# Kernel tuning notes

Hardware: AMD Instinct MI355X
Metric: run time of the kernel (lower is better)

The kernel has to match this reference:

```python
import jax, jax.numpy as jnp
import numpy as np

D = 1024
K = 8
EPS_BN = 1e-5
EPS_L2 = 1e-8


def l2norm(x, axis=-1):
    return x / (jnp.sqrt(jnp.sum(x * x, axis=axis, keepdims=True)) + EPS_L2)


def setup_inputs() -> dict:
    key = jax.random.key(0)
    ks = jax.random.split(key, 12)
    B, T = 256, 72
    H = D // K
    s1 = 1.0 / np.sqrt(D)
    s2 = 1.0 / np.sqrt(H)
    return {
        "img_embed": jax.random.normal(ks[0], (B, 36, D), dtype=jnp.float32),
        "cap_embed": jax.random.normal(ks[1], (B, T, D), dtype=jnp.float32),
        "lens": jax.random.randint(ks[2], (B,), 1, T + 1),
        # fc_gamma: Linear(D,H) -> ReLU -> Linear(H,D); weights stored (in,out)
        "Wg1": jax.random.uniform(ks[3], (D, H), jnp.float32, -s1, s1),
        "bg1": jax.random.uniform(ks[4], (H,), jnp.float32, -s1, s1),
        "Wg2": jax.random.uniform(ks[5], (H, D), jnp.float32, -s2, s2),
        "bg2": jax.random.uniform(ks[6], (D,), jnp.float32, -s2, s2),
        # fc_beta
        "Wb1": jax.random.uniform(ks[7], (D, H), jnp.float32, -s1, s1),
        "bb1": jax.random.uniform(ks[8], (H,), jnp.float32, -s1, s1),
        "Wb2": jax.random.uniform(ks[9], (H, D), jnp.float32, -s2, s2),
        "bb2": jax.random.uniform(ks[10], (D,), jnp.float32, -s2, s2),
    }


def reference(img_embed, cap_embed, lens, Wg1, bg1, Wg2, bg2, Wb1, bb1, Wb2, bb2):
    # img_embed: (B, 36, D), cap_embed: (B, T, D), lens: (B,)
    B, T, _ = cap_embed.shape

    # img_repr: mean over 36 regions -> (B, D)
    img_repr = img_embed.mean(axis=1)

    # BatchNorm1d (affine=False, training): stats over (batch, time) per feature.
    # cap in torch is (B, D, T); stats reduce over batch+time axes.
    mean = cap_embed.mean(axis=(0, 1))                      # (D,)
    var = jnp.mean((cap_embed - mean) ** 2, axis=(0, 1))    # biased, (D,)
    norm_feat = (cap_embed - mean) / jnp.sqrt(var + EPS_BN)  # (B, T, D)

    # Masked mean pooling over valid timesteps (BN stats precede masking,
    # matching the original). Pooling is linear, so conditional affine
    # (gamma,beta constant over time) commutes with it.
    mask = (jnp.arange(T)[None, :] < lens[:, None]).astype(cap_embed.dtype)  # (B, T)
    pooled = jnp.einsum('btd,bt->bd', norm_feat, mask) / lens[:, None].astype(cap_embed.dtype)  # (B_cap, D)

    # Conditional gamma/beta per image
    gammas = jax.nn.relu(img_repr @ Wg1 + bg1) @ Wg2 + bg2   # (B_img, D)
    betas = jax.nn.relu(img_repr @ Wb1 + bb1) @ Wb2 + bb2    # (B_img, D)

    # txt[i, j, :] = pooled[j] * (gamma_i + 1) + beta_i
    txt = pooled[None, :, :] * (gammas[:, None, :] + 1.0) + betas[:, None, :]  # (B_img, B_cap, D)
    txt_n = l2norm(txt, axis=-1)
    img_n = l2norm(img_repr, axis=-1)                        # (B_img, D)

    # sim for image i over captions j; original writes sims[:, i] = sim
    sim_ij = jnp.einsum('id,ijd->ij', img_n, txt_n)          # (B_img, B_cap)
    return sim_ij.T                                          # sims[j, i]
```

## Files before the change

### kernel.cpp

```cpp
#include <hip/hip_runtime.h>
#include <math.h>

#define NDIM 1024
#define HDIM 128
#define NB 256
#define NT 72
#define NR 36
#define KS 16

__device__ __forceinline__ float wave_sum(float v) {
#pragma unroll
  for (int off = 32; off > 0; off >>= 1) v += __shfl_down(v, off, 64);
  return v;
}

__device__ __forceinline__ float dot4(const float4 a, const float4 b) {
  return a.x * b.x + a.y * b.y + a.z * b.z + a.w * b.w;
}

__global__ __launch_bounds__(256) void k_front(const float* __restrict__ img,
                                               const float* __restrict__ cap,
                                               const int* __restrict__ lens,
                                               float* __restrict__ fs, float* __restrict__ fq,
                                               float* __restrict__ ms, float* __restrict__ repr,
                                               float* __restrict__ imgn) {
  const int bid = blockIdx.x, tid = threadIdx.x;
  __shared__ float red[4];
  __shared__ float sInv;
  if (bid < 512) {
    const int b = bid & 255;
    const int half = bid >> 8;
    const int len = lens[b];
    const int t0 = half * 36;
    const float* base = cap + (size_t)b * NT * NDIM + (size_t)t0 * NDIM + tid * 4;
    float fsx = 0.f, fsy = 0.f, fsz = 0.f, fsw = 0.f;
    float fqx = 0.f, fqy = 0.f, fqz = 0.f, fqw = 0.f;
    float msx = 0.f, msy = 0.f, msz = 0.f, msw = 0.f;
#pragma unroll 12
    for (int tt = 0; tt < 36; ++tt) {
      const float4 v = *reinterpret_cast<const float4*>(base + tt * NDIM);
      fsx += v.x; fsy += v.y; fsz += v.z; fsw += v.w;
      fqx += v.x * v.x; fqy += v.y * v.y; fqz += v.z * v.z; fqw += v.w * v.w;
      if (t0 + tt < len) { msx += v.x; msy += v.y; msz += v.z; msw += v.w; }
    }
    const int o = (half * NB + b) * NDIM + tid * 4;
    *reinterpret_cast<float4*>(fs + o) = make_float4(fsx, fsy, fsz, fsw);
    *reinterpret_cast<float4*>(fq + o) = make_float4(fqx, fqy, fqz, fqw);
    *reinterpret_cast<float4*>(ms + o) = make_float4(msx, msy, msz, msw);
  } else {
    const int b = bid - 512;
    const float* base = img + (size_t)b * NR * NDIM + tid * 4;
    float sx = 0.f, sy = 0.f, sz = 0.f, sw = 0.f;
#pragma unroll 12
    for (int r = 0; r < NR; ++r) {
      const float4 v = *reinterpret_cast<const float4*>(base + r * NDIM);
      sx += v.x; sy += v.y; sz += v.z; sw += v.w;
    }
    const float inv = 1.0f / (float)NR;
    sx *= inv; sy *= inv; sz *= inv; sw *= inv;
    *reinterpret_cast<float4*>(repr + (size_t)b * NDIM + tid * 4) = make_float4(sx, sy, sz, sw);
    const float sq = wave_sum(sx * sx + sy * sy + sz * sz + sw * sw);
    const int lane = tid & 63, wv = tid >> 6;
    if (lane == 0) red[wv] = sq;
    __syncthreads();
    if (tid == 0) sInv = 1.0f / (sqrtf(red[0] + red[1] + red[2] + red[3]) + 1e-8f);
    __syncthreads();
    const float iv = sInv;
    *reinterpret_cast<float4*>(imgn + (size_t)b * NDIM + tid * 4) =
        make_float4(sx * iv, sy * iv, sz * iv, sw * iv);
  }
}

__global__ __launch_bounds__(512) void k_mid(const float* __restrict__ fs,
                                             const float* __restrict__ fq,
                                             const float* __restrict__ ms,
                                             const int* __restrict__ lens,
                                             const float* __restrict__ repr,
                                             const float* __restrict__ Wg1,
                                             const float* __restrict__ Wb1,
                                             float* __restrict__ pooled,
                                             float* __restrict__ hpart) {
  const int bid = blockIdx.x, tid = threadIdx.x;
  __shared__ float ss[8][64], sq2[8][64], smu[64], srs[64];
  __shared__ float shr[8][128];
  __shared__ float sacc[8][128][8];
  if (bid < 16) {
    const int d0 = bid * 64, dloc = tid & 63, grp = tid >> 6;
    float s = 0.f, q = 0.f;
    const int r0 = grp * 64;
#pragma unroll 8
    for (int r = r0; r < r0 + 64; ++r) {
      s += fs[(size_t)r * NDIM + d0 + dloc];
      q += fq[(size_t)r * NDIM + d0 + dloc];
    }
    ss[grp][dloc] = s;
    sq2[grp][dloc] = q;
    __syncthreads();
    if (tid < 64) {
      float S = 0.f, Q = 0.f;
#pragma unroll
      for (int g2 = 0; g2 < 8; ++g2) { S += ss[g2][tid]; Q += sq2[g2][tid]; }
      const float invN = 1.0f / (float)(NB * NT);
      const float mu = S * invN;
      const float var = Q * invN - mu * mu;
      smu[tid] = mu;
      srs[tid] = 1.0f / sqrtf(var + 1e-5f);
    }
    __syncthreads();
    const int dcol = tid & 63, brow = tid >> 6;
    const float mu = smu[dcol], rs = srs[dcol];
#pragma unroll 4
    for (int b = brow; b < NB; b += 8) {
      const float invl = 1.0f / (float)lens[b];
      const float m = ms[(size_t)b * NDIM + d0 + dcol] + ms[(size_t)(NB + b) * NDIM + d0 + dcol];
      pooled[(size_t)b * NDIM + d0 + dcol] = (m * invl - mu) * rs;
    }
  } else {
    const int idx = bid - 16;
    const int g = idx & 31, br = (idx >> 5) & 1, ks = idx >> 6;
    const int b0 = g * 8;
    const int kbase = ks * 128;
    const int h2 = tid & 63;
    const int ksub = tid >> 6;
    const float* __restrict__ W = br ? Wb1 : Wg1;
    {
      const int im = tid >> 6, c2 = (tid & 63) * 2;
      *reinterpret_cast<float2*>(&shr[im][c2]) =
          *reinterpret_cast<const float2*>(repr + (size_t)(b0 + im) * NDIM + kbase + c2);
    }
    __syncthreads();
    float acc0[8] = {0, 0, 0, 0, 0, 0, 0, 0}, acc1[8] = {0, 0, 0, 0, 0, 0, 0, 0};
#pragma unroll
    for (int q = 0; q < 4; ++q) {
      const int dl = ksub * 16 + q * 4;
      const float* wq = W + (size_t)(kbase + dl) * HDIM + h2;
      const float wa0 = wq[0], wa1 = wq[128], wa2 = wq[256], wa3 = wq[384];
      const float wb0 = wq[64], wb1 = wq[192], wb2 = wq[320], wb3 = wq[448];
#pragma unroll
      for (int i = 0; i < 8; ++i) {
        const float4 s = *reinterpret_cast<const float4*>(&shr[i][dl]);
        acc0[i] += s.x * wa0 + s.y * wa1 + s.z * wa2 + s.w * wa3;
        acc1[i] += s.x * wb0 + s.y * wb1 + s.z * wb2 + s.w * wb3;
      }
    }
#pragma unroll
    for (int i = 0; i < 8; ++i) {
      sacc[ksub][h2][i] = acc0[i];
      sacc[ksub][h2 + 64][i] = acc1[i];
    }
    __syncthreads();
#pragma unroll
    for (int v = tid; v < 1024; v += 512) {
      const int hh = v & 127, im = v >> 7;
      float s = 0.f;
#pragma unroll
      for (int k2 = 0; k2 < 8; ++k2) s += sacc[k2][hh][im];
      hpart[(((size_t)ks * 2 + br) * NB + b0 + im) * HDIM + hh] = s;
    }
  }
}

__global__ __launch_bounds__(512) void k_l2(
    const float* __restrict__ hpart, const float* __restrict__ bg1,
    const float* __restrict__ bb1, const float* __restrict__ Wg2,
    const float* __restrict__ bg2, const float* __restrict__ Wb2,
    const float* __restrict__ bb2, const float* __restrict__ imgn, float* __restrict__ uarr,
    float* __restrict__ aarr, float* __restrict__ bvarr, float* __restrict__ cpart,
    float* __restrict__ epart) {
  const int gb = blockIdx.x, dgrp = blockIdx.y;
  const int b0 = gb * 8;
  const int tid = threadIdx.x;
  __shared__ float shh[2][8][HDIM];
  __shared__ float sga[8][HDIM];
  __shared__ float sba[8][HDIM];

  {
    const int hh4 = (tid & 31) * 4;
    const int imA = (tid >> 5) & 7;
    const int brA = tid >> 8;
    float4 acc = make_float4(0.f, 0.f, 0.f, 0.f);
    const float* hp = hpart + ((size_t)brA * NB + b0 + imA) * HDIM + hh4;
#pragma unroll
    for (int ks = 0; ks < 8; ++ks) {
      const float4 v = *reinterpret_cast<const float4*>(hp + (size_t)ks * 2 * NB * HDIM);
      acc.x += v.x; acc.y += v.y; acc.z += v.z; acc.w += v.w;
    }
    const float4 bias = *reinterpret_cast<const float4*>((brA ? bb1 : bg1) + hh4);
    *reinterpret_cast<float4*>(&shh[brA][imA][hh4]) =
        make_float4(fmaxf(acc.x + bias.x, 0.f), fmaxf(acc.y + bias.y, 0.f),
                    fmaxf(acc.z + bias.z, 0.f), fmaxf(acc.w + bias.w, 0.f));
  }
  __syncthreads();

  const int dq = tid & 31;
  const int im = (tid >> 5) & 7;
  const int hs = tid >> 8;
  const int d = dgrp * 128 + dq * 4;
  float4 ga = make_float4(0.f, 0.f, 0.f, 0.f), ba = make_float4(0.f, 0.f, 0.f, 0.f);
  const int h0 = hs * 64;
#pragma unroll 8
  for (int h = h0; h < h0 + 64; ++h) {
    const float4 wg = *reinterpret_cast<const float4*>(Wg2 + (size_t)h * NDIM + d);
    const float4 wb = *reinterpret_cast<const float4*>(Wb2 + (size_t)h * NDIM + d);
    const float hg = shh[0][im][h], hb = shh[1][im][h];
    ga.x += hg * wg.x; ga.y += hg * wg.y; ga.z += hg * wg.z; ga.w += hg * wg.w;
    ba.x += hb * wb.x; ba.y += hb * wb.y; ba.z += hb * wb.z; ba.w += hb * wb.w;
  }
  if (hs) {
    *reinterpret_cast<float4*>(&sga[im][dq * 4]) = ga;
    *reinterpret_cast<float4*>(&sba[im][dq * 4]) = ba;
  }
  __syncthreads();
  if (!hs) {
    const float4 g2 = *reinterpret_cast<const float4*>(&sga[im][dq * 4]);
    const float4 b2 = *reinterpret_cast<const float4*>(&sba[im][dq * 4]);
    const float4 bgv = *reinterpret_cast<const float4*>(bg2 + d);
    const float4 bbv = *reinterpret_cast<const float4*>(bb2 + d);
    const float ox = ga.x + g2.x + bgv.x + 1.0f, oy = ga.y + g2.y + bgv.y + 1.0f;
    const float oz = ga.z + g2.z + bgv.z + 1.0f, ow = ga.w + g2.w + bgv.w + 1.0f;
    const float tx = ba.x + b2.x + bbv.x, ty = ba.y + b2.y + bbv.y;
    const float tz = ba.z + b2.z + bbv.z, tw = ba.w + b2.w + bbv.w;
    const size_t o = (size_t)(b0 + im) * NDIM + d;
    const float4 nv = *reinterpret_cast<const float4*>(imgn + o);
    *reinterpret_cast<float4*>(uarr + o) = make_float4(nv.x * ox, nv.y * oy, nv.z * oz, nv.w * ow);
    *reinterpret_cast<float4*>(aarr + o) = make_float4(ox * ox, oy * oy, oz * oz, ow * ow);
    *reinterpret_cast<float4*>(bvarr + o) =
        make_float4(2.0f * ox * tx, 2.0f * oy * ty, 2.0f * oz * tz, 2.0f * ow * tw);
    float c = nv.x * tx + nv.y * ty + nv.z * tz + nv.w * tw;
    float e = tx * tx + ty * ty + tz * tz + tw * tw;
#pragma unroll
    for (int off = 16; off > 0; off >>= 1) {
      c += __shfl_down(c, off, 32);
      e += __shfl_down(e, off, 32);
    }
    if ((tid & 31) == 0) {
      cpart[dgrp * NB + b0 + im] = c;
      epart[dgrp * NB + b0 + im] = e;
    }
  }
}

__global__ __launch_bounds__(256) void k_simtile(
    const float* __restrict__ uarr, const float* __restrict__ aarr,
    const float* __restrict__ bvarr, const float* __restrict__ pooled,
    float* __restrict__ pn, float* __restrict__ pd) {
  __shared__ float su[64][36], sa[64][36], sb[64][36], sp[64][36];
  const int tid = threadIdx.x;
  const int tx = tid & 15, ty = tid >> 4;
  const int i0 = blockIdx.x * 64, j0 = blockIdx.y * 64;
  const int k0 = blockIdx.z * (NDIM / KS);
  const int lr = tid >> 3;
  const int lc = (tid & 7) * 4;
  float an[4][4] = {{0}}, ad[4][4] = {{0}};
  for (int dc = k0; dc < k0 + NDIM / KS; dc += 32) {
    __syncthreads();
#pragma unroll
    for (int rep = 0; rep < 2; ++rep) {
      const int r = lr + rep * 32;
      *reinterpret_cast<float4*>(&su[r][lc]) =
          *reinterpret_cast<const float4*>(uarr + (size_t)(i0 + r) * NDIM + dc + lc);
      *reinterpret_cast<float4*>(&sa[r][lc]) =
          *reinterpret_cast<const float4*>(aarr + (size_t)(i0 + r) * NDIM + dc + lc);
      *reinterpret_cast<float4*>(&sb[r][lc]) =
          *reinterpret_cast<const float4*>(bvarr + (size_t)(i0 + r) * NDIM + dc + lc);
      *reinterpret_cast<float4*>(&sp[r][lc]) =
          *reinterpret_cast<const float4*>(pooled + (size_t)(j0 + r) * NDIM + dc + lc);
    }
    __syncthreads();
#pragma unroll
    for (int dd = 0; dd < 32; dd += 4) {
      float4 rp[4], rq[4];
#pragma unroll
      for (int n = 0; n < 4; ++n) {
        rp[n] = *reinterpret_cast<const float4*>(&sp[ty + 16 * n][dd]);
        rq[n] = make_float4(rp[n].x * rp[n].x, rp[n].y * rp[n].y, rp[n].z * rp[n].z,
                            rp[n].w * rp[n].w);
      }
#pragma unroll
      for (int m = 0; m < 4; ++m) {
        const float4 ru = *reinterpret_cast<const float4*>(&su[tx + 16 * m][dd]);
        const float4 ra = *reinterpret_cast<const float4*>(&sa[tx + 16 * m][dd]);
        const float4 rb = *reinterpret_cast<const float4*>(&sb[tx + 16 * m][dd]);
#pragma unroll
        for (int n = 0; n < 4; ++n) {
          an[m][n] += dot4(ru, rp[n]);
          ad[m][n] += dot4(ra, rq[n]) + dot4(rb, rp[n]);
        }
      }
    }
  }
  const int s = blockIdx.z;
#pragma unroll
  for (int m = 0; m < 4; ++m) {
#pragma unroll
    for (int n = 0; n < 4; ++n) {
      const int i = i0 + tx + 16 * m, j = j0 + ty + 16 * n;
      const size_t o = ((size_t)s * NB + j) * NB + i;
      pn[o] = an[m][n];
      pd[o] = ad[m][n];
    }
  }
}

__global__ __launch_bounds__(256) void k_reduce(const float* __restrict__ pn,
                                                const float* __restrict__ pd,
                                                const float* __restrict__ cpart,
                                                const float* __restrict__ epart,
                                                float* __restrict__ out) {
  const int j = blockIdx.x, i = threadIdx.x;
  const size_t base = (size_t)j * NB + i;
  float n = 0.f, den = 0.f;
#pragma unroll
  for (int s = 0; s < KS; ++s) {
    const size_t o = base + (size_t)s * (NB * NB);
    n += pn[o];
    den += pd[o];
  }
  float cv = 0.f, ev = 0.f;
#pragma unroll
  for (int s = 0; s < 8; ++s) { cv += cpart[s * NB + i]; ev += epart[s * NB + i]; }
  const float num = n + cv;
  const float den2 = den + ev;
  out[base] = num / (sqrtf(fmaxf(den2, 0.0f)) + 1e-8f);
}

extern "C" void kernel_launch(void* const* d_in, const int* in_sizes, int n_in,
                              void* d_out, int out_size, void* d_ws, size_t ws_size,
                              hipStream_t stream) {
  const float* img = (const float*)d_in[0];
  const float* cap = (const float*)d_in[1];
  const int* lens = (const int*)d_in[2];
  const float* Wg1 = (const float*)d_in[3];
  const float* bg1 = (const float*)d_in[4];
  const float* Wg2 = (const float*)d_in[5];
  const float* bg2 = (const float*)d_in[6];
  const float* Wb1 = (const float*)d_in[7];
  const float* bb1 = (const float*)d_in[8];
  const float* Wb2 = (const float*)d_in[9];
  const float* bb2 = (const float*)d_in[10];
  float* out = (float*)d_out;

  float* w = (float*)d_ws;
  float* fullsum = w; w += 2 * NB * NDIM;
  float* fullsq = w;  w += 2 * NB * NDIM;
  float* msum = w;    w += 2 * NB * NDIM;
  float* hpart = w;   w += 16 * NB * HDIM;
  float* pooled = w;  w += NB * NDIM;
  float* uarr = w;    w += NB * NDIM;
  float* aarr = w;    w += NB * NDIM;
  float* bvarr = w;   w += NB * NDIM;
  float* cpart = w;   w += 8 * NB;
  float* epart = w;   w += 8 * NB;
  float* repr = uarr;
  float* imgn = aarr;
  float* pn = fullsum;
  float* pd = msum;

  hipLaunchKernelGGL(k_front, dim3(768), dim3(256), 0, stream, img, cap, lens, fullsum, fullsq,
                     msum, repr, imgn);
  hipLaunchKernelGGL(k_mid, dim3(528), dim3(512), 0, stream, fullsum, fullsq, msum, lens, repr,
                     Wg1, Wb1, pooled, hpart);
  hipLaunchKernelGGL(k_l2, dim3(32, 8), dim3(512), 0, stream, hpart, bg1, bb1, Wg2, bg2, Wb2,
                     bb2, imgn, uarr, aarr, bvarr, cpart, epart);
  hipLaunchKernelGGL(k_simtile, dim3(4, 4, KS), dim3(256), 0, stream, uarr, aarr, bvarr, pooled,
                     pn, pd);
  hipLaunchKernelGGL(k_reduce, dim3(NB), dim3(256), 0, stream, pn, pd, cpart, epart, out);
}
```

Baseline: 76.07 us.

## Reuse second-layer weights across images and retile the similarity kernel with fewer K-splits

The second MLP layer is restructured so each thread loads one weight float4 and applies it to all 8 images of the block. Partial sums over 8 h-segments are reduced through shared memory, which cuts repeated Wg2/Wb2 global loads. The similarity kernel now uses 32x32 tiles with 4 K-splits instead of 64x64 tiles with 16. This keeps the same block count but shrinks the partial-sum buffers the final reduce must read, at the cost of lower register reuse per thread. repr/imgn get their own workspace instead of aliasing uarr/aarr.

```diff
diff --git a/kernel.cpp b/kernel.cpp
--- a/kernel.cpp
+++ b/kernel.cpp
@@ -6,7 +6,7 @@
 #define NB 256
 #define NT 72
 #define NR 36
-#define KS 16
+#define KS 4
 
 __device__ __forceinline__ float wave_sum(float v) {
 #pragma unroll
@@ -171,8 +171,7 @@
   const int b0 = gb * 8;
   const int tid = threadIdx.x;
   __shared__ float shh[2][8][HDIM];
-  __shared__ float sga[8][HDIM];
-  __shared__ float sba[8][HDIM];
+  __shared__ float sacc[2][8][8][HDIM];
 
   {
     const int hh4 = (tid & 31) * 4;
@@ -192,50 +191,59 @@
   }
   __syncthreads();
 
-  const int dq = tid & 31;
-  const int im = (tid >> 5) & 7;
-  const int hs = tid >> 8;
-  const int d = dgrp * 128 + dq * 4;
-  float4 ga = make_float4(0.f, 0.f, 0.f, 0.f), ba = make_float4(0.f, 0.f, 0.f, 0.f);
-  const int h0 = hs * 64;
-#pragma unroll 8
-  for (int h = h0; h < h0 + 64; ++h) {
-    const float4 wg = *reinterpret_cast<const float4*>(Wg2 + (size_t)h * NDIM + d);
-    const float4 wb = *reinterpret_cast<const float4*>(Wb2 + (size_t)h * NDIM + d);
-    const float hg = shh[0][im][h], hb = shh[1][im][h];
-    ga.x += hg * wg.x; ga.y += hg * wg.y; ga.z += hg * wg.z; ga.w += hg * wg.w;
-    ba.x += hb * wb.x; ba.y += hb * wb.y; ba.z += hb * wb.z; ba.w += hb * wb.w;
-  }
-  if (hs) {
-    *reinterpret_cast<float4*>(&sga[im][dq * 4]) = ga;
-    *reinterpret_cast<float4*>(&sba[im][dq * 4]) = ba;
+  {
+    const int dq = tid & 31;
+    const int kseg = (tid >> 5) & 7;
+    const int br = tid >> 8;
+    const int d = dgrp * 128 + dq * 4;
+    const float* __restrict__ W = br ? Wb2 : Wg2;
+    float4 acc[8];
+#pragma unroll
+    for (int im = 0; im < 8; ++im) acc[im] = make_float4(0.f, 0.f, 0.f, 0.f);
+    const int h0 = kseg * 16;
+#pragma unroll
+    for (int hh = 0; hh < 16; ++hh) {
+      const int h = h0 + hh;
+      const float4 w4 = *reinterpret_cast<const float4*>(W + (size_t)h * NDIM + d);
+#pragma unroll
+      for (int im = 0; im < 8; ++im) {
+        const float hv = shh[br][im][h];
+        acc[im].x += hv * w4.x; acc[im].y += hv * w4.y;
+        acc[im].z += hv * w4.z; acc[im].w += hv * w4.w;
+      }
+    }
+#pragma unroll
+    for (int im = 0; im < 8; ++im)
+      *reinterpret_cast<float4*>(&sacc[br][kseg][im][dq * 4]) = acc[im];
   }
   __syncthreads();
-  if (!hs) {
-    const float4 g2 = *reinterpret_cast<const float4*>(&sga[im][dq * 4]);
-    const float4 b2 = *reinterpret_cast<const float4*>(&sba[im][dq * 4]);
-    const float4 bgv = *reinterpret_cast<const float4*>(bg2 + d);
-    const float4 bbv = *reinterpret_cast<const float4*>(bb2 + d);
-    const float ox = ga.x + g2.x + bgv.x + 1.0f, oy = ga.y + g2.y + bgv.y + 1.0f;
-    const float oz = ga.z + g2.z + bgv.z + 1.0f, ow = ga.w + g2.w + bgv.w + 1.0f;
-    const float tx = ba.x + b2.x + bbv.x, ty = ba.y + b2.y + bbv.y;
-    const float tz = ba.z + b2.z + bbv.z, tw = ba.w + b2.w + bbv.w;
-    const size_t o = (size_t)(b0 + im) * NDIM + d;
-    const float4 nv = *reinterpret_cast<const float4*>(imgn + o);
-    *reinterpret_cast<float4*>(uarr + o) = make_float4(nv.x * ox, nv.y * oy, nv.z * oz, nv.w * ow);
-    *reinterpret_cast<float4*>(aarr + o) = make_float4(ox * ox, oy * oy, oz * oz, ow * ow);
-    *reinterpret_cast<float4*>(bvarr + o) =
-        make_float4(2.0f * ox * tx, 2.0f * oy * ty, 2.0f * oz * tz, 2.0f * ow * tw);
-    float c = nv.x * tx + nv.y * ty + nv.z * tz + nv.w * tw;
-    float e = tx * tx + ty * ty + tz * tz + tw * tw;
-#pragma unroll
-    for (int off = 16; off > 0; off >>= 1) {
-      c += __shfl_down(c, off, 32);
-      e += __shfl_down(e, off, 32);
-    }
-    if ((tid & 31) == 0) {
-      cpart[dgrp * NB + b0 + im] = c;
-      epart[dgrp * NB + b0 + im] = e;
+
+  {
+    const int imC = tid >> 6;
+    const int dl = (tid & 63) * 2;
+    float g0 = 0.f, g1 = 0.f, t0 = 0.f, t1 = 0.f;
+#pragma unroll
+    for (int ks = 0; ks < 8; ++ks) {
+      g0 += sacc[0][ks][imC][dl];
+      g1 += sacc[0][ks][imC][dl + 1];
+      t0 += sacc[1][ks][imC][dl];
+      t1 += sacc[1][ks][imC][dl + 1];
+    }
+    const int d = dgrp * 128 + dl;
+    const float2 bgv = *reinterpret_cast<const float2*>(bg2 + d);
+    const float2 bbv = *reinterpret_cast<const float2*>(bb2 + d);
+    const float ox0 = g0 + bgv.x + 1.0f, ox1 = g1 + bgv.y + 1.0f;
+    const float tb0 = t0 + bbv.x, tb1 = t1 + bbv.y;
+    const size_t o = (size_t)(b0 + imC) * NDIM + d;
+    const float2 nv = *reinterpret_cast<const float2*>(imgn + o);
+    *reinterpret_cast<float2*>(uarr + o) = make_float2(nv.x * ox0, nv.y * ox1);
+    *reinterpret_cast<float2*>(aarr + o) = make_float2(ox0 * ox0, ox1 * ox1);
+    *reinterpret_cast<float2*>(bvarr + o) = make_float2(2.0f * ox0 * tb0, 2.0f * ox1 * tb1);
+    const float c = wave_sum(nv.x * tb0 + nv.y * tb1);
+    const float e = wave_sum(tb0 * tb0 + tb1 * tb1);
+    if ((tid & 63) == 0) {
+      cpart[dgrp * NB + b0 + imC] = c;
+      epart[dgrp * NB + b0 + imC] = e;
     }
   }
 }
@@ -244,56 +252,52 @@
     const float* __restrict__ uarr, const float* __restrict__ aarr,
     const float* __restrict__ bvarr, const float* __restrict__ pooled,
     float* __restrict__ pn, float* __restrict__ pd) {
-  __shared__ float su[64][36], sa[64][36], sb[64][36], sp[64][36];
+  __shared__ float su[32][36], sa[32][36], sb[32][36], sp[32][36];
   const int tid = threadIdx.x;
   const int tx = tid & 15, ty = tid >> 4;
-  const int i0 = blockIdx.x * 64, j0 = blockIdx.y * 64;
+  const int i0 = blockIdx.x * 32, j0 = blockIdx.y * 32;
   const int k0 = blockIdx.z * (NDIM / KS);
   const int lr = tid >> 3;
   const int lc = (tid & 7) * 4;
-  float an[4][4] = {{0}}, ad[4][4] = {{0}};
+  const int s = blockIdx.z;
+  float an[2][2] = {{0.f, 0.f}, {0.f, 0.f}}, ad[2][2] = {{0.f, 0.f}, {0.f, 0.f}};
   for (int dc = k0; dc < k0 + NDIM / KS; dc += 32) {
     __syncthreads();
-#pragma unroll
-    for (int rep = 0; rep < 2; ++rep) {
-      const int r = lr + rep * 32;
-      *reinterpret_cast<float4*>(&su[r][lc]) =
-          *reinterpret_cast<const float4*>(uarr + (size_t)(i0 + r) * NDIM + dc + lc);
-      *reinterpret_cast<float4*>(&sa[r][lc]) =
-          *reinterpret_cast<const float4*>(aarr + (size_t)(i0 + r) * NDIM + dc + lc);
-      *reinterpret_cast<float4*>(&sb[r][lc]) =
-          *reinterpret_cast<const float4*>(bvarr + (size_t)(i0 + r) * NDIM + dc + lc);
-      *reinterpret_cast<float4*>(&sp[r][lc]) =
-          *reinterpret_cast<const float4*>(pooled + (size_t)(j0 + r) * NDIM + dc + lc);
-    }
+    *reinterpret_cast<float4*>(&su[lr][lc]) =
+        *reinterpret_cast<const float4*>(uarr + (size_t)(i0 + lr) * NDIM + dc + lc);
+    *reinterpret_cast<float4*>(&sa[lr][lc]) =
+        *reinterpret_cast<const float4*>(aarr + (size_t)(i0 + lr) * NDIM + dc + lc);
+    *reinterpret_cast<float4*>(&sb[lr][lc]) =
+        *reinterpret_cast<const float4*>(bvarr + (size_t)(i0 + lr) * NDIM + dc + lc);
+    *reinterpret_cast<float4*>(&sp[lr][lc]) =
+        *reinterpret_cast<const float4*>(pooled + (size_t)(j0 + lr) * NDIM + dc + lc);
     __syncthreads();
 #pragma unroll
     for (int dd = 0; dd < 32; dd += 4) {
-      float4 rp[4], rq[4];
-#pragma unroll
-      for (int n = 0; n < 4; ++n) {
+      float4 rp[2], rq[2];
+#pragma unroll
+      for (int n = 0; n < 2; ++n) {
         rp[n] = *reinterpret_cast<const float4*>(&sp[ty + 16 * n][dd]);
         rq[n] = make_float4(rp[n].x * rp[n].x, rp[n].y * rp[n].y, rp[n].z * rp[n].z,
                             rp[n].w * rp[n].w);
       }
 #pragma unroll
-      for (int m = 0; m < 4; ++m) {
+      for (int m = 0; m < 2; ++m) {
         const float4 ru = *reinterpret_cast<const float4*>(&su[tx + 16 * m][dd]);
         const float4 ra = *reinterpret_cast<const float4*>(&sa[tx + 16 * m][dd]);
         const float4 rb = *reinterpret_cast<const float4*>(&sb[tx + 16 * m][dd]);
 #pragma unroll
-        for (int n = 0; n < 4; ++n) {
+        for (int n = 0; n < 2; ++n) {
           an[m][n] += dot4(ru, rp[n]);
           ad[m][n] += dot4(ra, rq[n]) + dot4(rb, rp[n]);
         }
       }
     }
   }
-  const int s = blockIdx.z;
-#pragma unroll
-  for (int m = 0; m < 4; ++m) {
-#pragma unroll
-    for (int n = 0; n < 4; ++n) {
+#pragma unroll
+  for (int m = 0; m < 2; ++m) {
+#pragma unroll
+    for (int n = 0; n < 2; ++n) {
       const int i = i0 + tx + 16 * m, j = j0 + ty + 16 * n;
       const size_t o = ((size_t)s * NB + j) * NB + i;
       pn[o] = an[m][n];
@@ -319,9 +323,7 @@
   float cv = 0.f, ev = 0.f;
 #pragma unroll
   for (int s = 0; s < 8; ++s) { cv += cpart[s * NB + i]; ev += epart[s * NB + i]; }
-  const float num = n + cv;
-  const float den2 = den + ev;
-  out[base] = num / (sqrtf(fmaxf(den2, 0.0f)) + 1e-8f);
+  out[base] = (n + cv) / (sqrtf(fmaxf(den + ev, 0.0f)) + 1e-8f);
 }
 
 extern "C" void kernel_launch(void* const* d_in, const int* in_sizes, int n_in,
@@ -349,12 +351,12 @@
   float* uarr = w;    w += NB * NDIM;
   float* aarr = w;    w += NB * NDIM;
   float* bvarr = w;   w += NB * NDIM;
+  float* repr = w;    w += NB * NDIM;
+  float* imgn = w;    w += NB * NDIM;
   float* cpart = w;   w += 8 * NB;
   float* epart = w;   w += 8 * NB;
-  float* repr = uarr;
-  float* imgn = aarr;
   float* pn = fullsum;
-  float* pd = msum;
+  float* pd = fullsum + 262144;
 
   hipLaunchKernelGGL(k_front, dim3(768), dim3(256), 0, stream, img, cap, lens, fullsum, fullsq,
                      msum, repr, imgn);
@@ -362,7 +364,7 @@
                      Wg1, Wb1, pooled, hpart);
   hipLaunchKernelGGL(k_l2, dim3(32, 8), dim3(512), 0, stream, hpart, bg1, bb1, Wg2, bg2, Wb2,
                      bb2, imgn, uarr, aarr, bvarr, cpart, epart);
-  hipLaunchKernelGGL(k_simtile, dim3(4, 4, KS), dim3(256), 0, stream, uarr, aarr, bvarr, pooled,
+  hipLaunchKernelGGL(k_simtile, dim3(8, 8, KS), dim3(256), 0, stream, uarr, aarr, bvarr, pooled,
                      pn, pd);
   hipLaunchKernelGGL(k_reduce, dim3(NB), dim3(256), 0, stream, pn, pd, cpart, epart, out);
 }
```

New measurement: 70.03 us. -7.9%, faster.
